# Optimization experiments

Hardware: AMD Instinct MI355X
Metric: run time of the kernel (lower is better)

Reference implementation:

```python
import jax, jax.numpy as jnp
import numpy as np

D_MODEL = 1024
N_HEADS = 16
HEAD_DIM = D_MODEL // N_HEADS
EPS = 1e-6


def _phi(x):
    # elu(x) + 1 feature map
    return jax.nn.elu(x) + 1.0


def setup_inputs() -> dict:
    key = jax.random.key(0)
    ks = jax.random.split(key, 12)
    B, N, M = 4, 4096, 4096
    s = 1.0 / np.sqrt(D_MODEL)
    return {
        "queries": jax.random.normal(ks[0], (B, N, D_MODEL), jnp.float32),
        "keys": jax.random.normal(ks[1], (B, M, D_MODEL), jnp.float32),
        "values": jax.random.normal(ks[2], (B, M, D_MODEL), jnp.float32),
        "wq": jax.random.normal(ks[3], (D_MODEL, D_MODEL), jnp.float32) * s,
        "bq": jax.random.normal(ks[4], (D_MODEL,), jnp.float32) * s,
        "wk": jax.random.normal(ks[5], (D_MODEL, D_MODEL), jnp.float32) * s,
        "bk": jax.random.normal(ks[6], (D_MODEL,), jnp.float32) * s,
        "wv": jax.random.normal(ks[7], (D_MODEL, D_MODEL), jnp.float32) * s,
        "bv": jax.random.normal(ks[8], (D_MODEL,), jnp.float32) * s,
        "wo": jax.random.normal(ks[9], (D_MODEL, D_MODEL), jnp.float32) * s,
        "bo": jax.random.normal(ks[10], (D_MODEL,), jnp.float32) * s,
    }


def reference(queries, keys, values, wq, bq, wk, bk, wv, bv, wo, bo):
    B, N, _ = queries.shape
    M = keys.shape[1]
    H, Dh = N_HEADS, HEAD_DIM
    # projections + head split -> [B, H, seq, Dh]
    q = _phi((queries @ wq.T + bq).reshape(B, N, H, Dh).transpose(0, 2, 1, 3))
    k = _phi((keys @ wk.T + bk).reshape(B, M, H, Dh).transpose(0, 2, 1, 3))
    v = (values @ wv.T + bv).reshape(B, M, H, Dh).transpose(0, 2, 1, 3)
    # kv aggregation: [B,H,Dh,Dh]
    kv = jnp.einsum("bhmd,bhme->bhde", k, v)
    # normalizer: [B,H,Dh]
    z = k.sum(axis=2)
    num = jnp.einsum("bhnd,bhde->bhne", q, kv)
    den = jnp.einsum("bhnd,bhd->bhn", q, z)[..., None] + EPS
    out = (num / den).transpose(0, 2, 1, 3).reshape(B, N, H * Dh)
    return out @ wo.T + bo
```

## Files before the change

kernel.cpp:

```cpp
#include <hip/hip_runtime.h>

#define EPS 1e-6f

typedef __attribute__((ext_vector_type(8))) __bf16 bf16x8;
typedef __attribute__((ext_vector_type(4))) float f32x4;
typedef __attribute__((ext_vector_type(4))) unsigned short us4v;
typedef __attribute__((ext_vector_type(8))) unsigned short us8v;
typedef unsigned short us;

__device__ inline us f2bf(float f) {
  unsigned int u = __builtin_bit_cast(unsigned int, f);
  unsigned int r = (u + 0x7fffu + ((u >> 16) & 1u)) >> 16;
  return (us)r;
}
__device__ inline float bf2f(us s) {
  unsigned int u = ((unsigned int)s) << 16;
  return __builtin_bit_cast(float, u);
}

__device__ inline void gl_lds16(const us* g, us* l) {
  __builtin_amdgcn_global_load_lds(
      (const __attribute__((address_space(1))) unsigned int*)g,
      (__attribute__((address_space(3))) unsigned int*)l, 16, 0, 0);
}

__global__ __launch_bounds__(256) void conv_bf16(const float* __restrict__ s,
                                                 us* __restrict__ d) {
  int idx = blockIdx.x * 256 + threadIdx.x;
  size_t base = (size_t)idx * 8;
  float4 a = *(const float4*)(s + base);
  float4 b = *(const float4*)(s + base + 4);
  us8v o;
  o[0] = f2bf(a.x); o[1] = f2bf(a.y); o[2] = f2bf(a.z); o[3] = f2bf(a.w);
  o[4] = f2bf(b.x); o[5] = f2bf(b.y); o[6] = f2bf(b.z); o[7] = f2bf(b.w);
  *(us8v*)(d + base) = o;
}

template <int MODE>
__global__ __launch_bounds__(256) void proj_gemm(const us* __restrict__ X,
                                                 const us* __restrict__ W,
                                                 const float* __restrict__ bias,
                                                 void* __restrict__ Yv) {
  __shared__ alignas(16) us Xs[128 * 64];
  __shared__ alignas(16) us Ws[128 * 64];

  const int t = threadIdx.x;
  const int wave = t >> 6, lane = t & 63;
  const int q4 = lane >> 4, l16 = lane & 15;
  const int wm = wave & 1, wn = wave >> 1;
  const int bid = blockIdx.x;
  const int colBase = (bid >> 7) << 7;
  const int rowBase = (bid & 127) << 7;

  const int srow0 = t >> 3;
  const int spos = (t & 7) ^ (srow0 & 7);
  const us* Xg = X + (size_t)rowBase * 1024 + (size_t)srow0 * 1024 + spos * 8;
  const us* Wg = W + (size_t)colBase * 1024 + (size_t)srow0 * 1024 + spos * 8;

  f32x4 acc[4][4];
#pragma unroll
  for (int i = 0; i < 4; i++)
#pragma unroll
    for (int j = 0; j < 4; j++) acc[i][j] = (f32x4){0.f, 0.f, 0.f, 0.f};

  for (int k0 = 0; k0 < 1024; k0 += 64) {
#pragma unroll
    for (int i = 0; i < 4; i++) {
      gl_lds16(Xg + (size_t)i * 32 * 1024 + k0, &Xs[(i * 256 + wave * 64) * 8]);
      gl_lds16(Wg + (size_t)i * 32 * 1024 + k0, &Ws[(i * 256 + wave * 64) * 8]);
    }
    __syncthreads();

#pragma unroll
    for (int ks = 0; ks < 2; ks++) {
      bf16x8 af[4], bfr[4];
#pragma unroll
      for (int i = 0; i < 4; i++) {
        int r = wm * 64 + i * 16 + l16;
        af[i] = *(const bf16x8*)&Xs[r * 64 + ((((ks << 2) | q4)) ^ (r & 7)) * 8];
      }
#pragma unroll
      for (int j = 0; j < 4; j++) {
        int r = wn * 64 + j * 16 + l16;
        bfr[j] = *(const bf16x8*)&Ws[r * 64 + ((((ks << 2) | q4)) ^ (r & 7)) * 8];
      }
#pragma unroll
      for (int i = 0; i < 4; i++)
#pragma unroll
        for (int j = 0; j < 4; j++)
          acc[i][j] = __builtin_amdgcn_mfma_f32_16x16x32_bf16(af[i], bfr[j], acc[i][j], 0, 0, 0);
    }
    __syncthreads();
  }

#pragma unroll
  for (int j = 0; j < 4; j++) {
    int col = colBase + wn * 64 + j * 16 + l16;
    float bv = bias[col];
#pragma unroll
    for (int i = 0; i < 4; i++) {
      int row0 = rowBase + wm * 64 + i * 16 + q4 * 4;
      if (MODE == 1 || MODE == 2) {
        int b = row0 >> 12, m0 = row0 & 4095;
        int h = col >> 6, dd = col & 63;
        us4v pk;
#pragma unroll
        for (int r = 0; r < 4; r++) {
          float y = acc[i][j][r] + bv;
          if (MODE == 1) y = (y > 0.f) ? (y + 1.f) : __expf(y);
          pk[r] = f2bf(y);
        }
        *(us4v*)&((us*)Yv)[(((size_t)((b * 16 + h) * 64 + dd)) << 12) + m0] = pk;
      } else {
#pragma unroll
        for (int r = 0; r < 4; r++) {
          float y = acc[i][j][r] + bv;
          if (MODE == 0) {
            y = (y > 0.f) ? (y + 1.f) : __expf(y);
            ((us*)Yv)[(size_t)(row0 + r) * 1024 + col] = f2bf(y);
          } else {
            ((float*)Yv)[(size_t)(row0 + r) * 1024 + col] = y;
          }
        }
      }
    }
  }
}

__global__ __launch_bounds__(256) void kv_stage1(const us* __restrict__ kt,
                                                 const us* __restrict__ vt,
                                                 float* __restrict__ part,
                                                 float* __restrict__ zpart) {
  __shared__ float red[4][4096];
  __shared__ float zred[4][64][4];

  const int blk = blockIdx.x;
  const int bh = blk >> 2, split = blk & 3;
  const int t = threadIdx.x;
  const int w = t >> 6, lane = t & 63;
  const int q4 = lane >> 4, l16 = lane & 15;
  const us* ktb = kt + (size_t)bh * 64 * 4096;
  const us* vtb = vt + (size_t)bh * 64 * 4096;
  const int mbeg = split * 1024 + w * 256;

  f32x4 acc[4][4];
#pragma unroll
  for (int i = 0; i < 4; i++)
#pragma unroll
    for (int j = 0; j < 4; j++) acc[i][j] = (f32x4){0.f, 0.f, 0.f, 0.f};
  float zacc[4] = {0.f, 0.f, 0.f, 0.f};

  for (int m0 = mbeg; m0 < mbeg + 256; m0 += 32) {
    bf16x8 af[4], bfr[4];
#pragma unroll
    for (int i = 0; i < 4; i++)
      af[i] = *(const bf16x8*)&vtb[(size_t)(i * 16 + l16) * 4096 + m0 + q4 * 8];
#pragma unroll
    for (int j = 0; j < 4; j++) {
      us8v ub = *(const us8v*)&ktb[(size_t)(j * 16 + l16) * 4096 + m0 + q4 * 8];
      bfr[j] = __builtin_bit_cast(bf16x8, ub);
#pragma unroll
      for (int e = 0; e < 8; e++) zacc[j] += bf2f(ub[e]);
    }
#pragma unroll
    for (int i = 0; i < 4; i++)
#pragma unroll
      for (int j = 0; j < 4; j++)
        acc[i][j] = __builtin_amdgcn_mfma_f32_16x16x32_bf16(af[i], bfr[j], acc[i][j], 0, 0, 0);
  }

#pragma unroll
  for (int i = 0; i < 4; i++)
#pragma unroll
    for (int j = 0; j < 4; j++)
#pragma unroll
      for (int r = 0; r < 4; r++)
        red[w][(i * 16 + q4 * 4 + r) * 64 + j * 16 + l16] = acc[i][j][r];
#pragma unroll
  for (int j = 0; j < 4; j++) zred[w][j * 16 + l16][q4] = zacc[j];
  __syncthreads();

  float* pb = part + (size_t)blk * 4096;
#pragma unroll
  for (int i = 0; i < 16; i++) {
    int idx = t + 256 * i;
    pb[idx] = red[0][idx] + red[1][idx] + red[2][idx] + red[3][idx];
  }
  if (t < 64) {
    float s = 0.f;
#pragma unroll
    for (int w2 = 0; w2 < 4; w2++)
#pragma unroll
      for (int q = 0; q < 4; q++) s += zred[w2][t][q];
    zpart[blk * 64 + t] = s;
  }
}

__global__ __launch_bounds__(256) void kv_stage2(const float* __restrict__ part,
                                                 const float* __restrict__ zpart,
                                                 us* __restrict__ kvb,
                                                 float* __restrict__ z) {
  const int bh = blockIdx.x;
  const int t = threadIdx.x;
  const float* p0 = part + (size_t)bh * 4 * 4096;
#pragma unroll
  for (int i = 0; i < 16; i++) {
    int idx = t + 256 * i;
    float s = p0[idx] + p0[4096 + idx] + p0[8192 + idx] + p0[12288 + idx];
    kvb[(size_t)bh * 4096 + idx] = f2bf(s);
  }
  if (t < 64) {
    const float* zp = zpart + (size_t)bh * 4 * 64;
    z[bh * 64 + t] = zp[t] + zp[64 + t] + zp[128 + t] + zp[192 + t];
  }
}

__global__ __launch_bounds__(256) void attn_kernel(const us* __restrict__ q,
                                                   const us* __restrict__ kvb,
                                                   const float* __restrict__ z,
                                                   us* __restrict__ attn) {
  __shared__ alignas(16) us kvs[64 * 72];
  __shared__ float zs[64];
  __shared__ float invden[256];

  const int bid = blockIdx.x;
  const int bh = bid >> 4, nc = bid & 15;
  const int b = bh >> 4, h = bh & 15;
  const int n0 = nc * 256;
  const int t = threadIdx.x;
  const int wave = t >> 6, lane = t & 63;
  const int q4 = lane >> 4, l16 = lane & 15;

#pragma unroll
  for (int i = 0; i < 2; i++) {
    int chunk = t + 256 * i;
    int e = chunk >> 3, d8 = chunk & 7;
    us8v vv = *(const us8v*)&kvb[(size_t)bh * 4096 + chunk * 8];
    *(us8v*)&kvs[e * 72 + d8 * 8] = vv;
  }
  if (t < 64) zs[t] = z[bh * 64 + t];
  __syncthreads();

  {
    const us* qrow = q + ((size_t)(b * 4096 + n0 + t)) * 1024 + h * 64;
    float s = 0.f;
#pragma unroll
    for (int d0 = 0; d0 < 64; d0 += 8) {
      us8v v = *(const us8v*)(qrow + d0);
#pragma unroll
      for (int j = 0; j < 8; j++) s += bf2f(v[j]) * zs[d0 + j];
    }
    invden[t] = 1.0f / (s + EPS);
  }
  __syncthreads();

  f32x4 acc[4][4];
#pragma unroll
  for (int i = 0; i < 4; i++)
#pragma unroll
    for (int j = 0; j < 4; j++) acc[i][j] = (f32x4){0.f, 0.f, 0.f, 0.f};

  const us* qb = q + ((size_t)(b * 4096 + n0 + wave * 64)) * 1024 + h * 64;
#pragma unroll
  for (int ks = 0; ks < 2; ks++) {
    bf16x8 af[4], bfr[4];
#pragma unroll
    for (int i = 0; i < 4; i++)
      af[i] = *(const bf16x8*)(qb + (size_t)(i * 16 + l16) * 1024 + ks * 32 + q4 * 8);
#pragma unroll
    for (int j = 0; j < 4; j++)
      bfr[j] = *(const bf16x8*)&kvs[(j * 16 + l16) * 72 + ks * 32 + q4 * 8];
#pragma unroll
    for (int i = 0; i < 4; i++)
#pragma unroll
      for (int j = 0; j < 4; j++)
        acc[i][j] = __builtin_amdgcn_mfma_f32_16x16x32_bf16(af[i], bfr[j], acc[i][j], 0, 0, 0);
  }

  us* ab = attn + ((size_t)(b * 4096 + n0 + wave * 64)) * 1024 + h * 64;
#pragma unroll
  for (int i = 0; i < 4; i++)
#pragma unroll
    for (int j = 0; j < 4; j++)
#pragma unroll
      for (int r = 0; r < 4; r++) {
        int rowl = i * 16 + q4 * 4 + r;
        int nl = wave * 64 + rowl;
        int e = j * 16 + l16;
        ab[(size_t)rowl * 1024 + e] = f2bf(acc[i][j][r] * invden[nl]);
      }
}

extern "C" void kernel_launch(void* const* d_in, const int* in_sizes, int n_in,
                              void* d_out, int out_size, void* d_ws, size_t ws_size,
                              hipStream_t stream) {
  const float* queries = (const float*)d_in[0];
  const float* keys    = (const float*)d_in[1];
  const float* values  = (const float*)d_in[2];
  const float* wq = (const float*)d_in[3];
  const float* bq = (const float*)d_in[4];
  const float* wk = (const float*)d_in[5];
  const float* bk = (const float*)d_in[6];
  const float* wv = (const float*)d_in[7];
  const float* bv = (const float*)d_in[8];
  const float* wo = (const float*)d_in[9];
  const float* bo = (const float*)d_in[10];

  char* ws = (char*)d_ws;
  const size_t TB = (size_t)16384 * 1024 * 2;
  us* A   = (us*)(ws);
  us* Bb  = (us*)(ws + TB);
  us* Xb  = (us*)(ws + 2 * TB);
  us* wqb = (us*)(ws + 3 * TB);
  us* wkb = wqb + (size_t)1024 * 1024;
  us* wvb = wkb + (size_t)1024 * 1024;
  us* wob = wvb + (size_t)1024 * 1024;
  float* part  = (float*)(wob + (size_t)1024 * 1024);
  float* zpart = part + (size_t)256 * 4096;
  float* z     = zpart + 256 * 64;
  us* kvb      = (us*)(z + 4096);

  const int GRID_IN = 16384 * 1024 / 2048;
  const int GRID_W  = 1024 * 1024 / 2048;

  conv_bf16<<<GRID_W, 256, 0, stream>>>(wq, wqb);
  conv_bf16<<<GRID_W, 256, 0, stream>>>(wk, wkb);
  conv_bf16<<<GRID_W, 256, 0, stream>>>(wv, wvb);
  conv_bf16<<<GRID_W, 256, 0, stream>>>(wo, wob);

  conv_bf16<<<GRID_IN, 256, 0, stream>>>(keys, Xb);
  proj_gemm<1><<<1024, 256, 0, stream>>>(Xb, wkb, bk, (void*)A);
  conv_bf16<<<GRID_IN, 256, 0, stream>>>(values, Xb);
  proj_gemm<2><<<1024, 256, 0, stream>>>(Xb, wvb, bv, (void*)Bb);
  kv_stage1<<<256, 256, 0, stream>>>(A, Bb, part, zpart);
  kv_stage2<<<64, 256, 0, stream>>>(part, zpart, kvb, z);
  conv_bf16<<<GRID_IN, 256, 0, stream>>>(queries, Bb);
  proj_gemm<0><<<1024, 256, 0, stream>>>(Bb, wqb, bq, (void*)A);
  attn_kernel<<<1024, 256, 0, stream>>>(A, kvb, z, A);
  proj_gemm<3><<<1024, 256, 0, stream>>>(A, wob, bo, d_out);
}
```

Baseline: 467.6 us.

## Fuse fp32-to-bf16 conversion into projections and attention into Q projection epilogue

```diff
diff --git a/kernel.cpp b/kernel.cpp
--- a/kernel.cpp
+++ b/kernel.cpp
@@ -1,4 +1,5 @@
 #include <hip/hip_runtime.h>
+#include <hip/hip_bf16.h>
 
 #define EPS 1e-6f
 
@@ -6,6 +7,7 @@
 typedef __attribute__((ext_vector_type(4))) float f32x4;
 typedef __attribute__((ext_vector_type(4))) unsigned short us4v;
 typedef __attribute__((ext_vector_type(8))) unsigned short us8v;
+typedef __attribute__((ext_vector_type(4))) unsigned int ui4v;
 typedef unsigned short us;
 
 __device__ inline us f2bf(float f) {
@@ -16,6 +18,16 @@
 __device__ inline float bf2f(us s) {
   unsigned int u = ((unsigned int)s) << 16;
   return __builtin_bit_cast(float, u);
+}
+__device__ inline unsigned int pk2(float a, float b) {
+  if constexpr (sizeof(__hip_bfloat162) == 4) {
+    __hip_bfloat162 h = __float22bfloat162_rn(make_float2(a, b));
+    unsigned int u;
+    __builtin_memcpy(&u, &h, 4);
+    return u;
+  } else {
+    return (unsigned int)f2bf(a) | ((unsigned int)f2bf(b) << 16);
+  }
 }
 
 __device__ inline void gl_lds16(const us* g, us* l) {
@@ -30,19 +42,25 @@
   size_t base = (size_t)idx * 8;
   float4 a = *(const float4*)(s + base);
   float4 b = *(const float4*)(s + base + 4);
-  us8v o;
-  o[0] = f2bf(a.x); o[1] = f2bf(a.y); o[2] = f2bf(a.z); o[3] = f2bf(a.w);
-  o[4] = f2bf(b.x); o[5] = f2bf(b.y); o[6] = f2bf(b.z); o[7] = f2bf(b.w);
-  *(us8v*)(d + base) = o;
+  unsigned int p0 = pk2(a.x, a.y), p1 = pk2(a.z, a.w);
+  unsigned int p2 = pk2(b.x, b.y), p3 = pk2(b.z, b.w);
+  *(ui4v*)(d + base) = (ui4v){p0, p1, p2, p3};
 }
 
 template <int MODE>
-__global__ __launch_bounds__(256) void proj_gemm(const us* __restrict__ X,
+__global__ __launch_bounds__(256) void proj_gemm(const void* __restrict__ Xv,
                                                  const us* __restrict__ W,
                                                  const float* __restrict__ bias,
-                                                 void* __restrict__ Yv) {
-  __shared__ alignas(16) us Xs[128 * 64];
-  __shared__ alignas(16) us Ws[128 * 64];
+                                                 void* __restrict__ Yv,
+                                                 const us* __restrict__ kvb,
+                                                 const float* __restrict__ zg) {
+  constexpr int SMU = (MODE == 0) ? 25600 : 16384;
+  __shared__ alignas(16) us smem[SMU];
+  __shared__ float fbuf[(MODE == 0) ? 512 : 4];
+  us* Xs = smem;
+  us* Ws = smem + 8192;
+  us* tile = smem;
+  us* kvs = smem + 16384;
 
   const int t = threadIdx.x;
   const int wave = t >> 6, lane = t & 63;
@@ -51,11 +69,27 @@
   const int bid = blockIdx.x;
   const int colBase = (bid >> 7) << 7;
   const int rowBase = (bid & 127) << 7;
+  const int b = rowBase >> 12;
+
+  if (MODE == 0) {
+    const int h0 = colBase >> 6;
+    const size_t kvbase = ((size_t)(b * 16 + h0)) << 12;
+#pragma unroll
+    for (int i = 0; i < 4; i++) {
+      int c = t + 256 * i;
+      int head = c >> 9, rem = c & 511;
+      us8v v = *(const us8v*)&kvb[kvbase + ((size_t)head << 12) + rem * 8];
+      *(us8v*)&kvs[head * 4608 + (rem >> 3) * 72 + (rem & 7) * 8] = v;
+    }
+    if (t < 128) {
+      fbuf[256 + t] = zg[(b * 16 + h0 + (t >> 6)) * 64 + (t & 63)];
+      fbuf[384 + t] = bias[colBase + t];
+    }
+  }
 
   const int srow0 = t >> 3;
-  const int spos = (t & 7) ^ (srow0 & 7);
-  const us* Xg = X + (size_t)rowBase * 1024 + (size_t)srow0 * 1024 + spos * 8;
-  const us* Wg = W + (size_t)colBase * 1024 + (size_t)srow0 * 1024 + spos * 8;
+  const int spos8 = ((t & 7) ^ (srow0 & 7)) * 8;
+  const us* Wg = W + (size_t)(colBase + srow0) * 1024 + spos8;
 
   f32x4 acc[4][4];
 #pragma unroll
@@ -65,44 +99,76 @@
 
   for (int k0 = 0; k0 < 1024; k0 += 64) {
 #pragma unroll
-    for (int i = 0; i < 4; i++) {
-      gl_lds16(Xg + (size_t)i * 32 * 1024 + k0, &Xs[(i * 256 + wave * 64) * 8]);
+    for (int i = 0; i < 4; i++)
       gl_lds16(Wg + (size_t)i * 32 * 1024 + k0, &Ws[(i * 256 + wave * 64) * 8]);
+    if (MODE == 3) {
+      const us* Xg = (const us*)Xv + (size_t)(rowBase + srow0) * 1024 + spos8;
+#pragma unroll
+      for (int i = 0; i < 4; i++)
+        gl_lds16(Xg + (size_t)i * 32 * 1024 + k0, &Xs[(i * 256 + wave * 64) * 8]);
+    } else {
+      const float* Xf = (const float*)Xv;
+#pragma unroll
+      for (int i = 0; i < 4; i++) {
+        int g = t + 256 * i;
+        int r = g >> 3, c = g & 7;
+        const float* p = Xf + (size_t)(rowBase + r) * 1024 + k0 + c * 8;
+        float4 a = *(const float4*)p;
+        float4 bq = *(const float4*)(p + 4);
+        unsigned int p0 = pk2(a.x, a.y), p1 = pk2(a.z, a.w);
+        unsigned int p2 = pk2(bq.x, bq.y), p3 = pk2(bq.z, bq.w);
+        *(ui4v*)&Xs[r * 64 + ((c ^ (r & 7)) << 3)] = (ui4v){p0, p1, p2, p3};
+      }
     }
     __syncthreads();
 
 #pragma unroll
     for (int ks = 0; ks < 2; ks++) {
-      bf16x8 af[4], bfr[4];
+      bf16x8 xf[4], wf[4];
+#pragma unroll
+      for (int a = 0; a < 4; a++) {
+        int rr = wm * 64 + a * 16 + l16;
+        xf[a] = *(const bf16x8*)&Xs[rr * 64 + ((((ks << 2) | q4)) ^ (rr & 7)) * 8];
+      }
+#pragma unroll
+      for (int a = 0; a < 4; a++) {
+        int rr = wn * 64 + a * 16 + l16;
+        wf[a] = *(const bf16x8*)&Ws[rr * 64 + ((((ks << 2) | q4)) ^ (rr & 7)) * 8];
+      }
+#pragma unroll
+      for (int i = 0; i < 4; i++)
+#pragma unroll
+        for (int j = 0; j < 4; j++) {
+          if (MODE == 0)
+            acc[i][j] = __builtin_amdgcn_mfma_f32_16x16x32_bf16(wf[i], xf[j], acc[i][j], 0, 0, 0);
+          else
+            acc[i][j] = __builtin_amdgcn_mfma_f32_16x16x32_bf16(xf[i], wf[j], acc[i][j], 0, 0, 0);
+        }
+    }
+    __syncthreads();
+  }
+
+  if (MODE == 3) {
+#pragma unroll
+    for (int j = 0; j < 4; j++) {
+      int col = colBase + wn * 64 + j * 16 + l16;
+      float bv = bias[col];
 #pragma unroll
       for (int i = 0; i < 4; i++) {
-        int r = wm * 64 + i * 16 + l16;
-        af[i] = *(const bf16x8*)&Xs[r * 64 + ((((ks << 2) | q4)) ^ (r & 7)) * 8];
-      }
-#pragma unroll
-      for (int j = 0; j < 4; j++) {
-        int r = wn * 64 + j * 16 + l16;
-        bfr[j] = *(const bf16x8*)&Ws[r * 64 + ((((ks << 2) | q4)) ^ (r & 7)) * 8];
-      }
-#pragma unroll
-      for (int i = 0; i < 4; i++)
-#pragma unroll
-        for (int j = 0; j < 4; j++)
-          acc[i][j] = __builtin_amdgcn_mfma_f32_16x16x32_bf16(af[i], bfr[j], acc[i][j], 0, 0, 0);
-    }
-    __syncthreads();
-  }
-
-#pragma unroll
-  for (int j = 0; j < 4; j++) {
-    int col = colBase + wn * 64 + j * 16 + l16;
-    float bv = bias[col];
-#pragma unroll
-    for (int i = 0; i < 4; i++) {
-      int row0 = rowBase + wm * 64 + i * 16 + q4 * 4;
-      if (MODE == 1 || MODE == 2) {
-        int b = row0 >> 12, m0 = row0 & 4095;
-        int h = col >> 6, dd = col & 63;
+        int row0 = rowBase + wm * 64 + i * 16 + q4 * 4;
+#pragma unroll
+        for (int r = 0; r < 4; r++)
+          ((float*)Yv)[(size_t)(row0 + r) * 1024 + col] = acc[i][j][r] + bv;
+      }
+    }
+  } else if (MODE == 1 || MODE == 2) {
+#pragma unroll
+    for (int j = 0; j < 4; j++) {
+      int cl = wn * 64 + j * 16 + l16;
+      float bv = bias[colBase + cl];
+#pragma unroll
+      for (int i = 0; i < 4; i++) {
+        int m0 = wm * 64 + i * 16 + q4 * 4;
         us4v pk;
 #pragma unroll
         for (int r = 0; r < 4; r++) {
@@ -110,19 +176,99 @@
           if (MODE == 1) y = (y > 0.f) ? (y + 1.f) : __expf(y);
           pk[r] = f2bf(y);
         }
-        *(us4v*)&((us*)Yv)[(((size_t)((b * 16 + h) * 64 + dd)) << 12) + m0] = pk;
-      } else {
+        int cm = m0 >> 3, sub = (m0 >> 2) & 1;
+        *(us4v*)&tile[cl * 128 + ((cm ^ (cl & 15)) << 3) + sub * 4] = pk;
+      }
+    }
+    __syncthreads();
+#pragma unroll
+    for (int p = 0; p < 8; p++) {
+      int cl = p * 16 + (t >> 4);
+      int cm = t & 15;
+      us8v v = *(const us8v*)&tile[cl * 128 + ((cm ^ (cl & 15)) << 3)];
+      int gc = colBase + cl;
+      int h = gc >> 6, dd = gc & 63;
+      int m0g = (rowBase & 4095) + cm * 8;
+      *(us8v*)&((us*)Yv)[(((size_t)((b * 16 + h) * 64 + dd)) << 12) + m0g] = v;
+    }
+  } else {
+#pragma unroll
+    for (int i = 0; i < 4; i++) {
+      int c0 = wn * 64 + i * 16 + q4 * 4;
+      float4 bv = *(const float4*)&fbuf[384 + c0];
+      int cq = c0 >> 3, sub = (c0 >> 2) & 1;
+#pragma unroll
+      for (int j = 0; j < 4; j++) {
+        int nl = wm * 64 + j * 16 + l16;
+        us4v pk;
+        float bvr[4] = {bv.x, bv.y, bv.z, bv.w};
 #pragma unroll
         for (int r = 0; r < 4; r++) {
-          float y = acc[i][j][r] + bv;
-          if (MODE == 0) {
-            y = (y > 0.f) ? (y + 1.f) : __expf(y);
-            ((us*)Yv)[(size_t)(row0 + r) * 1024 + col] = f2bf(y);
-          } else {
-            ((float*)Yv)[(size_t)(row0 + r) * 1024 + col] = y;
-          }
+          float y = acc[i][j][r] + bvr[r];
+          y = (y > 0.f) ? (y + 1.f) : __expf(y);
+          pk[r] = f2bf(y);
         }
-      }
+        *(us4v*)&tile[nl * 128 + ((cq ^ (nl & 15)) << 3) + sub * 4] = pk;
+      }
+    }
+    __syncthreads();
+    {
+      int nl = t & 127, hh = t >> 7;
+      float s = 0.f;
+#pragma unroll
+      for (int c8 = 0; c8 < 8; c8++) {
+        int pos = (hh * 8 + c8) ^ (nl & 15);
+        us8v v = *(const us8v*)&tile[nl * 128 + (pos << 3)];
+#pragma unroll
+        for (int e = 0; e < 8; e++) s += bf2f(v[e]) * fbuf[256 + hh * 64 + c8 * 8 + e];
+      }
+      fbuf[hh * 128 + nl] = 1.0f / (s + EPS);
+    }
+    f32x4 a2[4][4];
+#pragma unroll
+    for (int i = 0; i < 4; i++)
+#pragma unroll
+      for (int j = 0; j < 4; j++) a2[i][j] = (f32x4){0.f, 0.f, 0.f, 0.f};
+#pragma unroll
+    for (int ks = 0; ks < 2; ks++) {
+      bf16x8 kf[4], qf[4];
+#pragma unroll
+      for (int a = 0; a < 4; a++)
+        kf[a] = *(const bf16x8*)&kvs[wn * 4608 + (a * 16 + l16) * 72 + ks * 32 + q4 * 8];
+#pragma unroll
+      for (int a = 0; a < 4; a++) {
+        int nl = wm * 64 + a * 16 + l16;
+        int cq = wn * 8 + ks * 4 + q4;
+        qf[a] = *(const bf16x8*)&tile[nl * 128 + ((cq ^ (nl & 15)) << 3)];
+      }
+#pragma unroll
+      for (int i = 0; i < 4; i++)
+#pragma unroll
+        for (int j = 0; j < 4; j++)
+          a2[i][j] = __builtin_amdgcn_mfma_f32_16x16x32_bf16(kf[i], qf[j], a2[i][j], 0, 0, 0);
+    }
+    __syncthreads();
+#pragma unroll
+    for (int i = 0; i < 4; i++) {
+      int c0 = wn * 64 + i * 16 + q4 * 4;
+      int cq = c0 >> 3, sub = (c0 >> 2) & 1;
+#pragma unroll
+      for (int j = 0; j < 4; j++) {
+        int nl = wm * 64 + j * 16 + l16;
+        float iv = fbuf[wn * 128 + nl];
+        us4v pk;
+#pragma unroll
+        for (int r = 0; r < 4; r++) pk[r] = f2bf(a2[i][j][r] * iv);
+        *(us4v*)&tile[nl * 128 + ((cq ^ (nl & 15)) << 3) + sub * 4] = pk;
+      }
+    }
+    __syncthreads();
+#pragma unroll
+    for (int p = 0; p < 8; p++) {
+      int nl = p * 16 + (t >> 4);
+      int cc = t & 15;
+      us8v v = *(const us8v*)&tile[nl * 128 + ((cc ^ (nl & 15)) << 3)];
+      *(us8v*)&((us*)Yv)[(size_t)(rowBase + nl) * 1024 + colBase + cc * 8] = v;
     }
   }
 }
@@ -135,13 +281,13 @@
   __shared__ float zred[4][64][4];
 
   const int blk = blockIdx.x;
-  const int bh = blk >> 2, split = blk & 3;
+  const int bh = blk >> 3, split = blk & 7;
   const int t = threadIdx.x;
   const int w = t >> 6, lane = t & 63;
   const int q4 = lane >> 4, l16 = lane & 15;
   const us* ktb = kt + (size_t)bh * 64 * 4096;
   const us* vtb = vt + (size_t)bh * 64 * 4096;
-  const int mbeg = split * 1024 + w * 256;
+  const int mbeg = split * 512 + w * 128;
 
   f32x4 acc[4][4];
 #pragma unroll
@@ -150,7 +296,7 @@
     for (int j = 0; j < 4; j++) acc[i][j] = (f32x4){0.f, 0.f, 0.f, 0.f};
   float zacc[4] = {0.f, 0.f, 0.f, 0.f};
 
-  for (int m0 = mbeg; m0 < mbeg + 256; m0 += 32) {
+  for (int m0 = mbeg; m0 < mbeg + 128; m0 += 32) {
     bf16x8 af[4], bfr[4];
 #pragma unroll
     for (int i = 0; i < 4; i++)
@@ -202,93 +348,22 @@
                                                  float* __restrict__ z) {
   const int bh = blockIdx.x;
   const int t = threadIdx.x;
-  const float* p0 = part + (size_t)bh * 4 * 4096;
+  const float* p0 = part + (size_t)bh * 8 * 4096;
 #pragma unroll
   for (int i = 0; i < 16; i++) {
     int idx = t + 256 * i;
-    float s = p0[idx] + p0[4096 + idx] + p0[8192 + idx] + p0[12288 + idx];
-    kvb[(size_t)bh * 4096 + idx] = f2bf(s);
+    float s = 0.f;
+#pragma unroll
+    for (int q = 0; q < 8; q++) s += p0[q * 4096 + idx];
+    kvb[((size_t)bh << 12) + idx] = f2bf(s);
   }
   if (t < 64) {
-    const float* zp = zpart + (size_t)bh * 4 * 64;
-    z[bh * 64 + t] = zp[t] + zp[64 + t] + zp[128 + t] + zp[192 + t];
-  }
-}
-
-__global__ __launch_bounds__(256) void attn_kernel(const us* __restrict__ q,
-                                                   const us* __restrict__ kvb,
-                                                   const float* __restrict__ z,
-                                                   us* __restrict__ attn) {
-  __shared__ alignas(16) us kvs[64 * 72];
-  __shared__ float zs[64];
-  __shared__ float invden[256];
-
-  const int bid = blockIdx.x;
-  const int bh = bid >> 4, nc = bid & 15;
-  const int b = bh >> 4, h = bh & 15;
-  const int n0 = nc * 256;
-  const int t = threadIdx.x;
-  const int wave = t >> 6, lane = t & 63;
-  const int q4 = lane >> 4, l16 = lane & 15;
-
-#pragma unroll
-  for (int i = 0; i < 2; i++) {
-    int chunk = t + 256 * i;
-    int e = chunk >> 3, d8 = chunk & 7;
-    us8v vv = *(const us8v*)&kvb[(size_t)bh * 4096 + chunk * 8];
-    *(us8v*)&kvs[e * 72 + d8 * 8] = vv;
-  }
-  if (t < 64) zs[t] = z[bh * 64 + t];
-  __syncthreads();
-
-  {
-    const us* qrow = q + ((size_t)(b * 4096 + n0 + t)) * 1024 + h * 64;
+    const float* zp = zpart + (size_t)bh * 8 * 64;
     float s = 0.f;
 #pragma unroll
-    for (int d0 = 0; d0 < 64; d0 += 8) {
-      us8v v = *(const us8v*)(qrow + d0);
-#pragma unroll
-      for (int j = 0; j < 8; j++) s += bf2f(v[j]) * zs[d0 + j];
-    }
-    invden[t] = 1.0f / (s + EPS);
-  }
-  __syncthreads();
-
-  f32x4 acc[4][4];
-#pragma unroll
-  for (int i = 0; i < 4; i++)
-#pragma unroll
-    for (int j = 0; j < 4; j++) acc[i][j] = (f32x4){0.f, 0.f, 0.f, 0.f};
-
-  const us* qb = q + ((size_t)(b * 4096 + n0 + wave * 64)) * 1024 + h * 64;
-#pragma unroll
-  for (int ks = 0; ks < 2; ks++) {
-    bf16x8 af[4], bfr[4];
-#pragma unroll
-    for (int i = 0; i < 4; i++)
-      af[i] = *(const bf16x8*)(qb + (size_t)(i * 16 + l16) * 1024 + ks * 32 + q4 * 8);
-#pragma unroll
-    for (int j = 0; j < 4; j++)
-      bfr[j] = *(const bf16x8*)&kvs[(j * 16 + l16) * 72 + ks * 32 + q4 * 8];
-#pragma unroll
-    for (int i = 0; i < 4; i++)
-#pragma unroll
-      for (int j = 0; j < 4; j++)
-        acc[i][j] = __builtin_amdgcn_mfma_f32_16x16x32_bf16(af[i], bfr[j], acc[i][j], 0, 0, 0);
-  }
-
-  us* ab = attn + ((size_t)(b * 4096 + n0 + wave * 64)) * 1024 + h * 64;
-#pragma unroll
-  for (int i = 0; i < 4; i++)
-#pragma unroll
-    for (int j = 0; j < 4; j++)
-#pragma unroll
-      for (int r = 0; r < 4; r++) {
-        int rowl = i * 16 + q4 * 4 + r;
-        int nl = wave * 64 + rowl;
-        int e = j * 16 + l16;
-        ab[(size_t)rowl * 1024 + e] = f2bf(acc[i][j][r] * invden[nl]);
-      }
+    for (int q = 0; q < 8; q++) s += zp[q * 64 + t];
+    z[bh * 64 + t] = s;
+  }
 }
 
 extern "C" void kernel_launch(void* const* d_in, const int* in_sizes, int n_in,
@@ -308,34 +383,29 @@
 
   char* ws = (char*)d_ws;
   const size_t TB = (size_t)16384 * 1024 * 2;
-  us* A   = (us*)(ws);
-  us* Bb  = (us*)(ws + TB);
-  us* Xb  = (us*)(ws + 2 * TB);
+  us* kt_buf   = (us*)(ws);
+  us* vt_buf   = (us*)(ws + TB);
+  us* attn_buf = (us*)(ws + 2 * TB);
+  float* part  = (float*)attn_buf;
+  float* zpart = part + (size_t)512 * 4096;
   us* wqb = (us*)(ws + 3 * TB);
   us* wkb = wqb + (size_t)1024 * 1024;
   us* wvb = wkb + (size_t)1024 * 1024;
   us* wob = wvb + (size_t)1024 * 1024;
-  float* part  = (float*)(wob + (size_t)1024 * 1024);
-  float* zpart = part + (size_t)256 * 4096;
-  float* z     = zpart + 256 * 64;
-  us* kvb      = (us*)(z + 4096);
-
-  const int GRID_IN = 16384 * 1024 / 2048;
-  const int GRID_W  = 1024 * 1024 / 2048;
+  us* kvb = wob + (size_t)1024 * 1024;
+  float* z = (float*)(kvb + (size_t)64 * 4096);
+
+  const int GRID_W = 1024 * 1024 / 2048;
 
   conv_bf16<<<GRID_W, 256, 0, stream>>>(wq, wqb);
   conv_bf16<<<GRID_W, 256, 0, stream>>>(wk, wkb);
   conv_bf16<<<GRID_W, 256, 0, stream>>>(wv, wvb);
   conv_bf16<<<GRID_W, 256, 0, stream>>>(wo, wob);
 
-  conv_bf16<<<GRID_IN, 256, 0, stream>>>(keys, Xb);
-  proj_gemm<1><<<1024, 256, 0, stream>>>(Xb, wkb, bk, (void*)A);
-  conv_bf16<<<GRID_IN, 256, 0, stream>>>(values, Xb);
-  proj_gemm<2><<<1024, 256, 0, stream>>>(Xb, wvb, bv, (void*)Bb);
-  kv_stage1<<<256, 256, 0, stream>>>(A, Bb, part, zpart);
+  proj_gemm<1><<<1024, 256, 0, stream>>>((const void*)keys, wkb, bk, (void*)kt_buf, nullptr, nullptr);
+  proj_gemm<2><<<1024, 256, 0, stream>>>((const void*)values, wvb, bv, (void*)vt_buf, nullptr, nullptr);
+  kv_stage1<<<512, 256, 0, stream>>>(kt_buf, vt_buf, part, zpart);
   kv_stage2<<<64, 256, 0, stream>>>(part, zpart, kvb, z);
-  conv_bf16<<<GRID_IN, 256, 0, stream>>>(queries, Bb);
-  proj_gemm<0><<<1024, 256, 0, stream>>>(Bb, wqb, bq, (void*)A);
-  attn_kernel<<<1024, 256, 0, stream>>>(A, kvb, z, A);
-  proj_gemm<3><<<1024, 256, 0, stream>>>(A, wob, bo, d_out);
-}
+  proj_gemm<0><<<1024, 256, 0, stream>>>((const void*)queries, wqb, bq, (void*)attn_buf, kvb, z);
+  proj_gemm<3><<<1024, 256, 0, stream>>>((const void*)attn_buf, wob, bo, d_out, nullptr, nullptr);
+}
```

Result: no change. 475.1 us (+1.6%).
